# Optimization experiments

Measured on AMD Instinct MI355X. Metric: run time of the kernel, lower is better.

Reference implementation:

```python
import jax, jax.numpy as jnp
import numpy as np

B, FC, FRAMES, C = 8, 256, 512, 256


def conv1d(x, w, stride=1, pad=(0, 0), dil=1):
    # x: [N, Cin, L], w: [Cout, Cin, K]
    return jax.lax.conv_general_dilated(
        x, w, window_strides=(stride,), padding=[pad],
        rhs_dilation=(dil,), dimension_numbers=('NCH', 'OIH', 'NCH'))


def setup_inputs() -> dict:
    key = jax.random.key(0)
    ks = jax.random.split(key, 8)
    s = 0.05
    x = jax.random.normal(ks[0], (B, FC, FRAMES), dtype=jnp.float32)
    enc_w0 = jax.random.normal(ks[1], (128, 1, 7), dtype=jnp.float32) * s
    enc_w123 = jax.random.normal(ks[2], (3, 128, 128, 7), dtype=jnp.float32) * s
    enc_w4567 = jax.random.normal(ks[3], (4, 128, 128, 3), dtype=jnp.float32) * s
    enc_w8 = jax.random.normal(ks[4], (C, 128, 1), dtype=jnp.float32) * s
    main_w = jax.random.normal(ks[5], (8, C, C, 2), dtype=jnp.float32) * s
    gate_w = jax.random.normal(ks[6], (8, C, C, 2), dtype=jnp.float32) * s
    judge_w = jax.random.normal(ks[7], (1, C, 1), dtype=jnp.float32) * s
    return {'x': x, 'enc_w0': enc_w0, 'enc_w123': enc_w123,
            'enc_w4567': enc_w4567, 'enc_w8': enc_w8,
            'main_w': main_w, 'gate_w': gate_w, 'judge_w': judge_w}


def reference(x, enc_w0, enc_w123, enc_w4567, enc_w8, main_w, gate_w, judge_w):
    lrelu = lambda h: jax.nn.leaky_relu(h, 0.2)
    b = x.shape[0]
    # [B, FC, FRAMES] -> [B*FRAMES, 1, FC]: encode each frame's feature vector
    h = jnp.transpose(x, (0, 2, 1)).reshape(-1, 1, FC)
    h = lrelu(conv1d(h, enc_w0, stride=2, pad=(3, 3)))
    for i in range(3):
        h = lrelu(conv1d(h, enc_w123[i], stride=2, pad=(3, 3)))
    for i in range(4):
        h = lrelu(conv1d(h, enc_w4567[i], stride=2, pad=(1, 1)))
    h = conv1d(h, enc_w8)                       # [B*FRAMES, C, 1], no activation
    h = jnp.transpose(h.reshape(b, FRAMES, C), (0, 2, 1))  # [B, C, FRAMES]
    # WaveNet stack: causal pad + dilated k=2 convs + tanh*sigmoid gate + residual
    feats = jnp.zeros_like(h)
    for i in range(8):
        p = 2 ** i
        z = jnp.tanh(conv1d(h, main_w[i], pad=(p, 0), dil=p)) * \
            jax.nn.sigmoid(conv1d(h, gate_w[i], pad=(p, 0), dil=p))
        feats = feats + z
        h = z + h                              # channels always match -> residual
    latent = feats
    j = conv1d(latent, judge_w)[:, :, -1:]      # [B, 1, 1]
    return latent[:, :, -1:], j
```

## Files before the change

kernel.cpp:

```cpp
#include <hip/hip_runtime.h>
#include <math.h>

#define FC 256
#define NB 8
#define RS 136

typedef __attribute__((ext_vector_type(8))) _Float16 f16x8;
typedef __attribute__((ext_vector_type(4))) float f32x4;

__device__ __forceinline__ float lrelu(float v) { return fmaxf(v, 0.2f * v); }
__device__ __forceinline__ unsigned short f2h(float f) {
  _Float16 h = (_Float16)f;
  return *(unsigned short*)&h;
}
__device__ __forceinline__ void bar() { asm volatile("s_barrier" ::: "memory"); }
__device__ __forceinline__ void wait_lgkm0() { asm volatile("s_waitcnt lgkmcnt(0)" ::: "memory"); }

#define N1 344064
#define N2 196608
#define N3 32768
#define NTOT 573440
#define NWN 2097152

__global__ void pack_kernel(const float* __restrict__ w123,
                            const float* __restrict__ w4567,
                            const float* __restrict__ w8,
                            const float* __restrict__ mw,
                            const float* __restrict__ gw,
                            unsigned short* __restrict__ wp,
                            unsigned short* __restrict__ wn) {
  int idx = blockIdx.x * 512 + threadIdx.x;
  if (idx < N1) {
    int e = idx & 7, lane = (idx >> 3) & 63, ct = (idx >> 9) & 7, ks = (idx >> 12) & 3, t = idx >> 14;
    int l = t / 7, kw = t % 7;
    int co = ct * 16 + (lane & 15), ci = ks * 32 + (lane >> 4) * 8 + e;
    wp[idx] = f2h(w123[(((l * 128 + co) * 128) + ci) * 7 + kw]);
  } else if (idx < N1 + N2) {
    int k = idx - N1;
    int e = k & 7, lane = (k >> 3) & 63, ct = (k >> 9) & 7, ks = (k >> 12) & 3, t = k >> 14;
    int l = t / 3, kw = t % 3;
    int co = ct * 16 + (lane & 15), ci = ks * 32 + (lane >> 4) * 8 + e;
    wp[idx] = f2h(w4567[(((l * 128 + co) * 128) + ci) * 3 + kw]);
  } else if (idx < NTOT) {
    int k = idx - N1 - N2;
    int e = k & 7, lane = (k >> 3) & 63, ct = (k >> 9) & 15, ks = (k >> 13) & 3;
    int co = ct * 16 + (lane & 15), ci = ks * 32 + (lane >> 4) * 8 + e;
    wp[idx] = f2h(w8[co * 128 + ci]);
  } else if (idx < NTOT + NWN) {
    int k2 = idx - NTOT;
    int li = k2 >> 18, w = k2 & 262143;
    int e = w & 7, lane = (w >> 3) & 63, rt = (w >> 9) & 31, k32 = w >> 14;
    int row = rt * 16 + (lane & 15), k = k32 * 32 + (lane >> 4) * 8 + e;
    int ch = row >> 1, mat = row & 1, kw = k >> 8, ci = k & 255;
    const float* src = mat ? gw : mw;
    wn[k2] = f2h(src[(((size_t)li * 256 + ch) * 256 + ci) * 2 + kw]);
  }
}

template<int KW, int POFF, int PIN, int POUT, int MC, int MN, int OM>
__device__ __forceinline__ void mlayer_d(const unsigned short* __restrict__ wp,
                                         const unsigned short* __restrict__ sin_,
                                         unsigned short* __restrict__ sout,
                                         unsigned short* __restrict__ gact,
                                         int tid, int frame) {
  constexpr int HRIN = PIN / 2 + 4;
  constexpr int HROUT = POUT / 2 + 4;
  constexpr int Nt = (POUT + 15) / 16;
  constexpr int MNg = Nt / MN;
  constexpr int MCg = 8 / MNg;
  static_assert(MC * MCg == 8, "cout tiling must cover 128 channels");
  constexpr int NS = KW * 4;
  constexpr int DA = NS < 6 ? NS : 6;
  constexpr int DB = MC == 1 ? (NS < 4 ? NS : 4) : (NS < 3 ? NS : 3);

  const int wid = tid >> 6, lane = tid & 63, nl = lane & 15, q = lane >> 4;
  const int mcg = wid / MNg, mng = wid % MNg;
  const int ct0 = mcg * MC, nt0 = mng * MN;

  int jj[MN]; bool val[MN]; int rofs[MN][KW];
#pragma unroll
  for (int jn = 0; jn < MN; ++jn) {
    int n = (nt0 + jn) * 16 + nl;
    val[jn] = (n < POUT);
    jj[jn] = val[jn] ? n : 0;
#pragma unroll
    for (int kw = 0; kw < KW; ++kw) {
      int P = 2 * jj[jn] + kw - POFF + 4;
      rofs[jn][kw] = ((P & 1) * HRIN + (P >> 1)) * RS + q * 8;
    }
  }
  const unsigned short* wl = wp + (size_t)ct0 * 512 + lane * 8;

  f32x4 acc[MC][MN];
#pragma unroll
  for (int i = 0; i < MC; ++i)
#pragma unroll
    for (int jn = 0; jn < MN; ++jn) acc[i][jn] = (f32x4){0.f, 0.f, 0.f, 0.f};

  f16x8 A[DA][MC], B[DB][MN];
#pragma unroll
  for (int s = 0; s < DA; ++s)
#pragma unroll
    for (int i = 0; i < MC; ++i)
      A[s][i] = *(const f16x8*)(wl + (size_t)s * 4096 + i * 512);
#pragma unroll
  for (int s = 0; s < DB; ++s) {
    const int kw = s >> 2, ks = s & 3;
#pragma unroll
    for (int jn = 0; jn < MN; ++jn)
      B[s][jn] = *(const f16x8*)(sin_ + rofs[jn][kw] + ks * 32);
  }
#pragma unroll
  for (int s = 0; s < NS; ++s) {
    const int sa = s % DA, sb = s % DB;
#pragma unroll
    for (int i = 0; i < MC; ++i)
#pragma unroll
      for (int jn = 0; jn < MN; ++jn)
        acc[i][jn] = __builtin_amdgcn_mfma_f32_16x16x32_f16(A[sa][i], B[sb][jn], acc[i][jn], 0, 0, 0);
    if (s + DA < NS) {
#pragma unroll
      for (int i = 0; i < MC; ++i)
        A[sa][i] = *(const f16x8*)(wl + (size_t)(s + DA) * 4096 + i * 512);
    }
    if (s + DB < NS) {
      const int kw = (s + DB) >> 2, ks = (s + DB) & 3;
#pragma unroll
      for (int jn = 0; jn < MN; ++jn)
        B[sb][jn] = *(const f16x8*)(sin_ + rofs[jn][kw] + ks * 32);
    }
  }

#pragma unroll
  for (int i = 0; i < MC; ++i) {
#pragma unroll
    for (int jn = 0; jn < MN; ++jn) {
      if (!val[jn]) continue;
      unsigned int lo = (unsigned)f2h(lrelu(acc[i][jn][0])) | ((unsigned)f2h(lrelu(acc[i][jn][1])) << 16);
      unsigned int hi = (unsigned)f2h(lrelu(acc[i][jn][2])) | ((unsigned)f2h(lrelu(acc[i][jn][3])) << 16);
      const int j = jj[jn];
      if (OM == 1) {
        *(uint2*)(gact + ((size_t)frame * POUT + j) * 128 + (ct0 + i) * 16 + q * 4) = make_uint2(lo, hi);
      } else {
        const int row = (j & 1) * HROUT + (j >> 1) + 2;
        *(uint2*)(sout + (size_t)row * RS + (ct0 + i) * 16 + q * 4) = make_uint2(lo, hi);
      }
    }
  }
  if (OM == 0) {
    constexpr int DEND = ((POUT - 1) >> 1) + 3;
    constexpr int NZ = 2 + (HROUT - DEND);
    unsigned int* zp = (unsigned int*)sout;
    for (int s2 = tid; s2 < 2 * NZ * 68; s2 += 512) {
      int col = s2 % 68, rr = s2 / 68;
      int par = rr / NZ, rz = rr % NZ;
      int row = rz < 2 ? rz : DEND + rz - 2;
      zp[((size_t)par * HROUT + row) * 68 + col] = 0;
    }
    __syncthreads();
  }
}

__global__ __launch_bounds__(512, 4)
void encoder1(const float* __restrict__ x, const float* __restrict__ w0,
              const unsigned short* __restrict__ wp123,
              const unsigned short* __restrict__ wp4,
              unsigned short* __restrict__ act4g) {
  __shared__ __align__(16) unsigned short actA[18496];
  __shared__ __align__(16) unsigned short actB[9792];
  float* s_x = (float*)actB;
  const int tid = threadIdx.x;
  const int frame = blockIdx.x;
  const int bb = frame >> 8;
  const int t = (frame & 255) + 256;

  if (tid < 256) s_x[3 + tid] = x[((bb << 8) + tid) * 512 + t];
  else if (tid < 259) s_x[tid - 256] = 0.f;
  else if (tid < 262) s_x[tid] = 0.f;
  wait_lgkm0();
  bar();

  {
    const int c = tid & 127;
    const int half = tid >> 7;
    float wv[7];
#pragma unroll
    for (int k = 0; k < 7; ++k) wv[k] = w0[c * 7 + k];
    for (int j = half * 32; j < half * 32 + 32; ++j) {
      float s = 0.f;
#pragma unroll
      for (int k = 0; k < 7; ++k) s += wv[k] * s_x[2 * j + k];
      int row = ((j & 1) ? 68 : 0) + (j >> 1) + 2;
      actA[row * RS + c] = f2h(lrelu(s));
    }
    unsigned int* zp = (unsigned int*)actA;
    for (int s2 = tid; s2 < 2 * 4 * 68; s2 += 512) {
      int col = s2 % 68;
      int rr = s2 / 68;
      int par = rr >> 2, r2 = rr & 3;
      int row = (r2 < 2) ? r2 : (64 + r2);
      zp[((size_t)par * 68 + row) * 68 + col] = 0;
    }
  }
  wait_lgkm0();
  bar();

  mlayer_d<7, 3, 128, 64, 2, 2, 0>(wp123,          actA, actB, nullptr, tid, frame);
  mlayer_d<7, 3, 64, 32, 1, 2, 0>(wp123 + 114688,  actB, actA, nullptr, tid, frame);
  mlayer_d<7, 3, 32, 16, 1, 1, 0>(wp123 + 229376,  actA, actA + 5440, nullptr, tid, frame);
  mlayer_d<3, 1, 16, 8, 1, 1, 1>(wp4,              actA + 5440, nullptr, act4g, tid, frame);
}

template<int KW, int POFF, int PIN, int POUT, int FPB, int COUT, int MC, int MN, int OM, bool FLATIN>
__device__ __forceinline__ void mlayer(const unsigned short* __restrict__ wp,
                                       const unsigned short* __restrict__ sin_,
                                       unsigned short* __restrict__ sout,
                                       float* __restrict__ gout,
                                       int tid, int frame0) {
  constexpr int HRIN  = PIN / 2 + 4;
  constexpr int HROUT = POUT / 2 + 4;
  constexpr int NVAL = POUT * FPB;
  constexpr int Nt = (NVAL + 15) / 16;
  constexpr int Ct = COUT / 16;
  constexpr int MCg = Ct / MC, MNg = Nt / MN;
  constexpr int KS = 4;
  constexpr int NS = KW * KS;
  constexpr int DA = NS < 6 ? NS : 6;
  constexpr int DB = NS < 3 ? NS : 3;
  constexpr int L2P = POUT == 1 ? 0 : POUT == 2 ? 1 : POUT == 4 ? 2 : POUT == 8 ? 3 :
                      POUT == 16 ? 4 : POUT == 32 ? 5 : 6;

  const int wid = tid >> 6, lane = tid & 63, nl = lane & 15, q = lane >> 4;

  for (int mac = wid; mac < MCg * MNg; mac += 8) {
    const int mcg = mac / MNg, mng = mac % MNg;
    const int ct0 = mcg * MC, nt0 = mng * MN;
    int jj[MN]; bool val[MN];
#pragma unroll
    for (int jn = 0; jn < MN; ++jn) {
      int n = (nt0 + jn) * 16 + nl;
      val[jn] = (n < NVAL);
      jj[jn] = val[jn] ? n : 0;
    }
    int rofs[MN][KW];
#pragma unroll
    for (int jn = 0; jn < MN; ++jn) {
      const int f = jj[jn] >> L2P, j = jj[jn] & (POUT - 1);
#pragma unroll
      for (int kw = 0; kw < KW; ++kw) {
        if (FLATIN) {
          rofs[jn][kw] = jj[jn] * RS + q * 8;
        } else {
          int P = 2 * j + kw - POFF + 4;
          rofs[jn][kw] = (f * 2 * HRIN + (P & 1) * HRIN + (P >> 1)) * RS + q * 8;
        }
      }
    }
    int abase[MC];
#pragma unroll
    for (int i = 0; i < MC; ++i) abase[i] = (ct0 + i) * 512 + lane * 8;

    f32x4 acc[MC][MN];
#pragma unroll
    for (int i = 0; i < MC; ++i)
#pragma unroll
      for (int jn = 0; jn < MN; ++jn) acc[i][jn] = (f32x4){0.f, 0.f, 0.f, 0.f};

    f16x8 A[DA][MC], B[DB][MN];
#pragma unroll
    for (int s = 0; s < DA; ++s) {
      const int kw = s / KS, ks = s % KS;
#pragma unroll
      for (int i = 0; i < MC; ++i)
        A[s][i] = *(const f16x8*)(wp + (size_t)(kw * KS + ks) * (Ct * 512) + abase[i]);
    }
#pragma unroll
    for (int s = 0; s < DB; ++s) {
      const int kw = s / KS, ks = s % KS;
#pragma unroll
      for (int jn = 0; jn < MN; ++jn)
        B[s][jn] = *(const f16x8*)(sin_ + rofs[jn][kw] + ks * 32);
    }
#pragma unroll
    for (int s = 0; s < NS; ++s) {
      const int sa = s % DA, sb = s % DB;
#pragma unroll
      for (int i = 0; i < MC; ++i)
#pragma unroll
        for (int jn = 0; jn < MN; ++jn)
          acc[i][jn] = __builtin_amdgcn_mfma_f32_16x16x32_f16(A[sa][i], B[sb][jn], acc[i][jn], 0, 0, 0);
      if (s + DA < NS) {
        const int kw = (s + DA) / KS, ks = (s + DA) % KS;
#pragma unroll
        for (int i = 0; i < MC; ++i)
          A[sa][i] = *(const f16x8*)(wp + (size_t)(kw * KS + ks) * (Ct * 512) + abase[i]);
      }
      if (s + DB < NS) {
        const int kw = (s + DB) / KS, ks = (s + DB) % KS;
#pragma unroll
        for (int jn = 0; jn < MN; ++jn)
          B[sb][jn] = *(const f16x8*)(sin_ + rofs[jn][kw] + ks * 32);
      }
    }
#pragma unroll
    for (int i = 0; i < MC; ++i) {
#pragma unroll
      for (int jn = 0; jn < MN; ++jn) {
        if (OM == 3) {
          if (val[jn]) {
            const int frame = frame0 + jj[jn];
            float4 v = make_float4(acc[i][jn][0], acc[i][jn][1], acc[i][jn][2], acc[i][jn][3]);
            *(float4*)(gout + (size_t)frame * 256 + (ct0 + i) * 16 + q * 4) = v;
          }
        } else if (OM == 2) {
          if (val[jn]) {
            unsigned int lo = (unsigned)f2h(lrelu(acc[i][jn][0])) | ((unsigned)f2h(lrelu(acc[i][jn][1])) << 16);
            unsigned int hi = (unsigned)f2h(lrelu(acc[i][jn][2])) | ((unsigned)f2h(lrelu(acc[i][jn][3])) << 16);
            *(uint2*)(sout + (size_t)jj[jn] * RS + (ct0 + i) * 16 + q * 4) = make_uint2(lo, hi);
          }
        } else {
          if (val[jn]) {
            const int f = jj[jn] >> L2P, j = jj[jn] & (POUT - 1);
            const int row = f * 2 * HROUT + (j & 1) * HROUT + (j >> 1) + 2;
            unsigned int lo = (unsigned)f2h(lrelu(acc[i][jn][0])) | ((unsigned)f2h(lrelu(acc[i][jn][1])) << 16);
            unsigned int hi = (unsigned)f2h(lrelu(acc[i][jn][2])) | ((unsigned)f2h(lrelu(acc[i][jn][3])) << 16);
            *(uint2*)(sout + (size_t)row * RS + (ct0 + i) * 16 + q * 4) = make_uint2(lo, hi);
          }
        }
      }
    }
  }
  if (OM == 0) {
    constexpr int DEND = ((POUT - 1) >> 1) + 3;
    constexpr int NZ = 2 + (HROUT - DEND);
    constexpr int TOTU = FPB * 2 * NZ * (RS / 2);
    unsigned int* zp = (unsigned int*)sout;
    for (int s2 = tid; s2 < TOTU; s2 += 512) {
      int col = s2 % 68;
      int rr = s2 / 68;
      int fr = rr / (2 * NZ), r2 = rr % (2 * NZ);
      int par = r2 / NZ, rz = r2 % NZ;
      int row = rz < 2 ? rz : DEND + rz - 2;
      zp[((size_t)(fr * 2 + par) * HROUT + row) * 68 + col] = 0;
    }
    __syncthreads();
  } else if (OM == 2) {
    __syncthreads();
  }
}

__global__ __launch_bounds__(512)
void encoder2(const unsigned short* __restrict__ act4g,
              const unsigned short* __restrict__ wp4,
              const unsigned short* __restrict__ wp8,
              float* __restrict__ h) {
  __shared__ __align__(16) unsigned short actP[17408];
  __shared__ __align__(16) unsigned short actQ[13056];
  __shared__ __align__(16) unsigned short actR[2176];
  const int tid = threadIdx.x;
  const int frame0 = blockIdx.x * 8;

  {
    uint4 z4 = make_uint4(0, 0, 0, 0);
    for (int s = tid; s < 2176; s += 512) ((uint4*)actP)[s] = z4;
    for (int s = tid; s < 1632; s += 512) ((uint4*)actQ)[s] = z4;
    for (int s = tid; s < 272; s += 512) ((uint4*)actR)[s] = z4;
  }
  __syncthreads();
  for (int c = tid; c < 1024; c += 512) {
    int f = c >> 7, rem = c & 127, pos = rem >> 4, o = (rem & 15) * 8;
    uint4 v = *(const uint4*)(act4g + ((size_t)(frame0 + f) * 8 + pos) * 128 + o);
    int P = pos + 4;
    int row = (P & 1) * 8 + (P >> 1);
    *(uint4*)(actP + ((size_t)f * 16 + row) * RS + o) = v;
  }
  __syncthreads();

  mlayer<3, 1, 8, 4, 8, 128, 2, 1, 0, false>(wp4 + 49152,  actP, actQ, nullptr, tid, frame0);
  mlayer<3, 1, 4, 2, 8, 128, 1, 1, 0, false>(wp4 + 98304,  actQ, actP, nullptr, tid, frame0);
  mlayer<3, 1, 2, 1, 8, 128, 1, 1, 2, false>(wp4 + 147456, actP, actR, nullptr, tid, frame0);
  mlayer<1, 0, 1, 1, 8, 256, 1, 1, 3, true>(wp8,           actR, nullptr, h, tid, frame0);
}

__global__ __launch_bounds__(256)
void wnet_kernel(const unsigned short* __restrict__ wn,
                 const float* __restrict__ hsrc, float* __restrict__ hdst,
                 float* __restrict__ feats, const float* __restrict__ jw,
                 float* __restrict__ out, int li) {
  const int npos = 128 >> li, p = 1 << li, N = npos * 8, lnp = 7 - li;
  const int tid = threadIdx.x;
  const int nb = blockIdx.x >> 2, mb = blockIdx.x & 3;
  const int n0 = nb * 16;
  __shared__ __align__(16) unsigned short sB[16 * 520];
  __shared__ float jls[8];

  for (int c = tid; c < 1024; c += 256) {
    const int nr = c >> 6, o = (c & 63) * 8;
    const int n = n0 + nr;
    unsigned short tmp[8] = {0, 0, 0, 0, 0, 0, 0, 0};
    if (n < N) {
      const int b = n >> lnp, kk = n & (npos - 1);
      const int t = 255 - (kk << (li + 1));
      const float* src = (o < 256) ? hsrc + ((size_t)(b * 256 + t - p)) * 256 + o
                                   : hsrc + ((size_t)(b * 256 + t)) * 256 + (o - 256);
#pragma unroll
      for (int e = 0; e < 8; ++e) tmp[e] = f2h(src[e]);
    }
    unsigned int u0 = (unsigned)tmp[0] | ((unsigned)tmp[1] << 16);
    unsigned int u1 = (unsigned)tmp[2] | ((unsigned)tmp[3] << 16);
    unsigned int u2 = (unsigned)tmp[4] | ((unsigned)tmp[5] << 16);
    unsigned int u3 = (unsigned)tmp[6] | ((unsigned)tmp[7] << 16);
    *(uint4*)(sB + (size_t)nr * 520 + o) = make_uint4(u0, u1, u2, u3);
  }
  __syncthreads();

  const int wid = tid >> 6, lane = tid & 63, nl = lane & 15, q = lane >> 4;
  f32x4 acc[2];
  acc[0] = (f32x4){0.f, 0.f, 0.f, 0.f};
  acc[1] = (f32x4){0.f, 0.f, 0.f, 0.f};
  int arow[2];
#pragma unroll
  for (int i = 0; i < 2; ++i) arow[i] = (mb * 8 + wid * 2 + i) * 512 + lane * 8;
  const int bofs = nl * 520 + q * 8;

  f16x8 A[4][2], Bv[2];
#pragma unroll
  for (int s = 0; s < 4; ++s)
#pragma unroll
    for (int i = 0; i < 2; ++i) A[s][i] = *(const f16x8*)(wn + arow[i] + (size_t)s * 16384);
#pragma unroll
  for (int s = 0; s < 2; ++s) Bv[s] = *(const f16x8*)(sB + bofs + s * 32);
#pragma unroll
  for (int s = 0; s < 16; ++s) {
    const int sa = s & 3, sb = s & 1;
    acc[0] = __builtin_amdgcn_mfma_f32_16x16x32_f16(A[sa][0], Bv[sb], acc[0], 0, 0, 0);
    acc[1] = __builtin_amdgcn_mfma_f32_16x16x32_f16(A[sa][1], Bv[sb], acc[1], 0, 0, 0);
    if (s + 4 < 16) {
#pragma unroll
      for (int i = 0; i < 2; ++i) A[sa][i] = *(const f16x8*)(wn + arow[i] + (size_t)(s + 4) * 16384);
    }
    if (s + 2 < 16) Bv[sb] = *(const f16x8*)(sB + bofs + (s + 2) * 32);
  }

  const int n = n0 + nl;
  if (li < 7) {
    if (n < N) {
      const int b = n >> lnp, kk = n & (npos - 1);
      const int t = 255 - (kk << (li + 1));
      const size_t rowoff = ((size_t)(b * 256 + t)) * 256;
#pragma unroll
      for (int i = 0; i < 2; ++i) {
        const int ch = mb * 64 + (wid * 2 + i) * 8 + q * 2;
        const float z0 = tanhf(acc[i][0]) * (1.f / (1.f + expf(-acc[i][1])));
        const float z1 = tanhf(acc[i][2]) * (1.f / (1.f + expf(-acc[i][3])));
        float2 hv = *(const float2*)(hsrc + rowoff + ch);
        *(float2*)(hdst + rowoff + ch) = make_float2(hv.x + z0, hv.y + z1);
        if (kk == 0) {
          float* fp = feats + b * 256 + ch;
          if (li == 0) { fp[0] = z0; fp[1] = z1; }
          else         { fp[0] += z0; fp[1] += z1; }
        }
      }
    }
  } else {
    if (tid < 8) jls[tid] = 0.f;
    __syncthreads();
    if (n < N) {
      const int b = n;
      float partial = 0.f;
#pragma unroll
      for (int i = 0; i < 2; ++i) {
        const int ch = mb * 64 + (wid * 2 + i) * 8 + q * 2;
        const float z0 = tanhf(acc[i][0]) * (1.f / (1.f + expf(-acc[i][1])));
        const float z1 = tanhf(acc[i][2]) * (1.f / (1.f + expf(-acc[i][3])));
        const float* fp = feats + b * 256 + ch;
        const float f0 = fp[0] + z0;
        const float f1 = fp[1] + z1;
        *(float2*)(out + b * 256 + ch) = make_float2(f0, f1);
        partial += f0 * jw[ch] + f1 * jw[ch + 1];
      }
      atomicAdd(&jls[b], partial);
    }
    __syncthreads();
    if (tid < 8) atomicAdd(out + NB * 256 + tid, jls[tid]);
  }
}

extern "C" void kernel_launch(void* const* d_in, const int* in_sizes, int n_in,
                              void* d_out, int out_size, void* d_ws, size_t ws_size,
                              hipStream_t stream) {
  const float* x     = (const float*)d_in[0];
  const float* w0    = (const float*)d_in[1];
  const float* w123  = (const float*)d_in[2];
  const float* w4567 = (const float*)d_in[3];
  const float* w8    = (const float*)d_in[4];
  const float* mw    = (const float*)d_in[5];
  const float* gw    = (const float*)d_in[6];
  const float* jw    = (const float*)d_in[7];
  float* out = (float*)d_out;

  float* ws = (float*)d_ws;
  unsigned short* act4g = (unsigned short*)ws;
  float* h0    = ws + 1048576;
  float* h1    = ws + 1572864;
  float* feats = ws + 2097152;
  unsigned short* wp = (unsigned short*)(ws + 2099200);
  unsigned short* wn = (unsigned short*)(ws + 2385920);

  hipMemsetAsync(out + NB * 256, 0, NB * sizeof(float), stream);
  pack_kernel<<<5216, 512, 0, stream>>>(w123, w4567, w8, mw, gw, wp, wn);
  encoder1<<<2048, 512, 0, stream>>>(x, w0, wp, wp + N1, act4g);
  encoder2<<<256, 512, 0, stream>>>(act4g, wp + N1, wp + N1 + N2, h0);

  float* hs = h0; float* hd = h1;
  for (int i = 0; i < 8; ++i) {
    const unsigned short* wl = wn + (size_t)i * 262144;
    const int N = (128 >> i) * 8;
    const int nN = (N + 15) / 16;
    wnet_kernel<<<4 * nN, 256, 0, stream>>>(wl, hs, hd, feats, jw, out, i);
    float* tmp = hd; hd = hs; hs = tmp;
  }
}
```

Baseline: 218.3 us.

## Process two frames per encoder1 block to reuse weight fragments

encoder1 now handles two frames per block. Each weight A-fragment loaded from global memory feeds MFMAs for both frames, and the LDS activation buffers are doubled. The grid is halved and launch bounds are dropped to 2 blocks per CU, which trades occupancy and more registers for halved weight traffic. Separately, the wnet_kernel staging loop now reads its input with float4 vector loads instead of scalar loads.

```diff
diff --git a/kernel.cpp b/kernel.cpp
--- a/kernel.cpp
+++ b/kernel.cpp
@@ -58,11 +58,13 @@
 }
 
 template<int KW, int POFF, int PIN, int POUT, int MC, int MN, int OM>
-__device__ __forceinline__ void mlayer_d(const unsigned short* __restrict__ wp,
-                                         const unsigned short* __restrict__ sin_,
-                                         unsigned short* __restrict__ sout,
-                                         unsigned short* __restrict__ gact,
-                                         int tid, int frame) {
+__device__ __forceinline__ void mlayer_d2(const unsigned short* __restrict__ wp,
+                                          const unsigned short* __restrict__ sin0,
+                                          const unsigned short* __restrict__ sin1,
+                                          unsigned short* __restrict__ sout0,
+                                          unsigned short* __restrict__ sout1,
+                                          unsigned short* __restrict__ gact,
+                                          int tid, int frame0) {
   constexpr int HRIN = PIN / 2 + 4;
   constexpr int HROUT = POUT / 2 + 4;
   constexpr int Nt = (POUT + 15) / 16;
@@ -71,11 +73,14 @@
   static_assert(MC * MCg == 8, "cout tiling must cover 128 channels");
   constexpr int NS = KW * 4;
   constexpr int DA = NS < 6 ? NS : 6;
-  constexpr int DB = MC == 1 ? (NS < 4 ? NS : 4) : (NS < 3 ? NS : 3);
+  constexpr int DB = NS < 3 ? NS : 3;
 
   const int wid = tid >> 6, lane = tid & 63, nl = lane & 15, q = lane >> 4;
   const int mcg = wid / MNg, mng = wid % MNg;
   const int ct0 = mcg * MC, nt0 = mng * MN;
+
+  const unsigned short* sins[2] = {sin0, sin1};
+  unsigned short* souts[2] = {sout0, sout1};
 
   int jj[MN]; bool val[MN]; int rofs[MN][KW];
 #pragma unroll
@@ -91,13 +96,15 @@
   }
   const unsigned short* wl = wp + (size_t)ct0 * 512 + lane * 8;
 
-  f32x4 acc[MC][MN];
+  f32x4 acc[MC][MN][2];
 #pragma unroll
   for (int i = 0; i < MC; ++i)
 #pragma unroll
-    for (int jn = 0; jn < MN; ++jn) acc[i][jn] = (f32x4){0.f, 0.f, 0.f, 0.f};
-
-  f16x8 A[DA][MC], B[DB][MN];
+    for (int jn = 0; jn < MN; ++jn)
+#pragma unroll
+      for (int f = 0; f < 2; ++f) acc[i][jn][f] = (f32x4){0.f, 0.f, 0.f, 0.f};
+
+  f16x8 A[DA][MC], B[DB][MN][2];
 #pragma unroll
   for (int s = 0; s < DA; ++s)
 #pragma unroll
@@ -108,7 +115,9 @@
     const int kw = s >> 2, ks = s & 3;
 #pragma unroll
     for (int jn = 0; jn < MN; ++jn)
-      B[s][jn] = *(const f16x8*)(sin_ + rofs[jn][kw] + ks * 32);
+#pragma unroll
+      for (int f = 0; f < 2; ++f)
+        B[s][jn][f] = *(const f16x8*)(sins[f] + rofs[jn][kw] + ks * 32);
   }
 #pragma unroll
   for (int s = 0; s < NS; ++s) {
@@ -117,7 +126,9 @@
     for (int i = 0; i < MC; ++i)
 #pragma unroll
       for (int jn = 0; jn < MN; ++jn)
-        acc[i][jn] = __builtin_amdgcn_mfma_f32_16x16x32_f16(A[sa][i], B[sb][jn], acc[i][jn], 0, 0, 0);
+#pragma unroll
+        for (int f = 0; f < 2; ++f)
+          acc[i][jn][f] = __builtin_amdgcn_mfma_f32_16x16x32_f16(A[sa][i], B[sb][jn][f], acc[i][jn][f], 0, 0, 0);
     if (s + DA < NS) {
 #pragma unroll
       for (int i = 0; i < MC; ++i)
@@ -127,88 +138,111 @@
       const int kw = (s + DB) >> 2, ks = (s + DB) & 3;
 #pragma unroll
       for (int jn = 0; jn < MN; ++jn)
-        B[sb][jn] = *(const f16x8*)(sin_ + rofs[jn][kw] + ks * 32);
-    }
-  }
-
-#pragma unroll
-  for (int i = 0; i < MC; ++i) {
-#pragma unroll
-    for (int jn = 0; jn < MN; ++jn) {
-      if (!val[jn]) continue;
-      unsigned int lo = (unsigned)f2h(lrelu(acc[i][jn][0])) | ((unsigned)f2h(lrelu(acc[i][jn][1])) << 16);
-      unsigned int hi = (unsigned)f2h(lrelu(acc[i][jn][2])) | ((unsigned)f2h(lrelu(acc[i][jn][3])) << 16);
-      const int j = jj[jn];
-      if (OM == 1) {
-        *(uint2*)(gact + ((size_t)frame * POUT + j) * 128 + (ct0 + i) * 16 + q * 4) = make_uint2(lo, hi);
-      } else {
-        const int row = (j & 1) * HROUT + (j >> 1) + 2;
-        *(uint2*)(sout + (size_t)row * RS + (ct0 + i) * 16 + q * 4) = make_uint2(lo, hi);
+#pragma unroll
+        for (int f = 0; f < 2; ++f)
+          B[sb][jn][f] = *(const f16x8*)(sins[f] + rofs[jn][kw] + ks * 32);
+    }
+  }
+
+#pragma unroll
+  for (int f = 0; f < 2; ++f) {
+#pragma unroll
+    for (int i = 0; i < MC; ++i) {
+#pragma unroll
+      for (int jn = 0; jn < MN; ++jn) {
+        if (!val[jn]) continue;
+        unsigned int lo = (unsigned)f2h(lrelu(acc[i][jn][f][0])) | ((unsigned)f2h(lrelu(acc[i][jn][f][1])) << 16);
+        unsigned int hi = (unsigned)f2h(lrelu(acc[i][jn][f][2])) | ((unsigned)f2h(lrelu(acc[i][jn][f][3])) << 16);
+        const int j = jj[jn];
+        if (OM == 1) {
+          *(uint2*)(gact + ((size_t)(frame0 + f) * POUT + j) * 128 + (ct0 + i) * 16 + q * 4) = make_uint2(lo, hi);
+        } else {
+          const int row = (j & 1) * HROUT + (j >> 1) + 2;
+          *(uint2*)(souts[f] + (size_t)row * RS + (ct0 + i) * 16 + q * 4) = make_uint2(lo, hi);
+        }
       }
     }
   }
   if (OM == 0) {
     constexpr int DEND = ((POUT - 1) >> 1) + 3;
     constexpr int NZ = 2 + (HROUT - DEND);
-    unsigned int* zp = (unsigned int*)sout;
-    for (int s2 = tid; s2 < 2 * NZ * 68; s2 += 512) {
-      int col = s2 % 68, rr = s2 / 68;
-      int par = rr / NZ, rz = rr % NZ;
-      int row = rz < 2 ? rz : DEND + rz - 2;
-      zp[((size_t)par * HROUT + row) * 68 + col] = 0;
+#pragma unroll
+    for (int f = 0; f < 2; ++f) {
+      unsigned int* zp = (unsigned int*)souts[f];
+      for (int s2 = tid; s2 < 2 * NZ * 68; s2 += 512) {
+        int col = s2 % 68, rr = s2 / 68;
+        int par = rr / NZ, rz = rr % NZ;
+        int row = rz < 2 ? rz : DEND + rz - 2;
+        zp[((size_t)par * HROUT + row) * 68 + col] = 0;
+      }
     }
     __syncthreads();
   }
 }
 
-__global__ __launch_bounds__(512, 4)
+__global__ __launch_bounds__(512, 2)
 void encoder1(const float* __restrict__ x, const float* __restrict__ w0,
               const unsigned short* __restrict__ wp123,
               const unsigned short* __restrict__ wp4,
               unsigned short* __restrict__ act4g) {
-  __shared__ __align__(16) unsigned short actA[18496];
-  __shared__ __align__(16) unsigned short actB[9792];
-  float* s_x = (float*)actB;
+  __shared__ __align__(16) unsigned short actA[2 * 18496];
+  __shared__ __align__(16) unsigned short actB[2 * 9792];
   const int tid = threadIdx.x;
-  const int frame = blockIdx.x;
-  const int bb = frame >> 8;
-  const int t = (frame & 255) + 256;
-
-  if (tid < 256) s_x[3 + tid] = x[((bb << 8) + tid) * 512 + t];
-  else if (tid < 259) s_x[tid - 256] = 0.f;
-  else if (tid < 262) s_x[tid] = 0.f;
+  const int frame0 = blockIdx.x * 2;
+  const int bb = frame0 >> 8;
+  const int t0 = (frame0 & 255) + 256;
+
+  float* s_x0 = (float*)actB;
+  float* s_x1 = (float*)actB + 272;
+
+  if (tid < 256) s_x0[3 + tid] = x[((bb << 8) + tid) * 512 + t0];
+  else           s_x1[3 + (tid & 255)] = x[((bb << 8) + (tid & 255)) * 512 + t0 + 1];
+  if (tid < 3)                 { s_x0[tid] = 0.f; s_x1[tid] = 0.f; }
+  if (tid >= 259 && tid < 262) { s_x0[tid] = 0.f; s_x1[tid] = 0.f; }
   wait_lgkm0();
   bar();
 
   {
     const int c = tid & 127;
-    const int half = tid >> 7;
+    const int sel = tid >> 7;
     float wv[7];
 #pragma unroll
     for (int k = 0; k < 7; ++k) wv[k] = w0[c * 7 + k];
-    for (int j = half * 32; j < half * 32 + 32; ++j) {
-      float s = 0.f;
-#pragma unroll
-      for (int k = 0; k < 7; ++k) s += wv[k] * s_x[2 * j + k];
-      int row = ((j & 1) ? 68 : 0) + (j >> 1) + 2;
-      actA[row * RS + c] = f2h(lrelu(s));
-    }
-    unsigned int* zp = (unsigned int*)actA;
-    for (int s2 = tid; s2 < 2 * 4 * 68; s2 += 512) {
-      int col = s2 % 68;
-      int rr = s2 / 68;
-      int par = rr >> 2, r2 = rr & 3;
-      int row = (r2 < 2) ? r2 : (64 + r2);
-      zp[((size_t)par * 68 + row) * 68 + col] = 0;
+#pragma unroll
+    for (int f = 0; f < 2; ++f) {
+      const float* sx = f ? s_x1 : s_x0;
+      unsigned short* aA = actA + f * 18496;
+      for (int j = sel * 32; j < sel * 32 + 32; ++j) {
+        float s = 0.f;
+#pragma unroll
+        for (int k = 0; k < 7; ++k) s += wv[k] * sx[2 * j + k];
+        int row = ((j & 1) ? 68 : 0) + (j >> 1) + 2;
+        aA[row * RS + c] = f2h(lrelu(s));
+      }
+    }
+#pragma unroll
+    for (int f = 0; f < 2; ++f) {
+      unsigned int* zp = (unsigned int*)(actA + f * 18496);
+      for (int s2 = tid; s2 < 2 * 4 * 68; s2 += 512) {
+        int col = s2 % 68;
+        int rr = s2 / 68;
+        int par = rr >> 2, r2 = rr & 3;
+        int row = (r2 < 2) ? r2 : (64 + r2);
+        zp[((size_t)par * 68 + row) * 68 + col] = 0;
+      }
     }
   }
   wait_lgkm0();
   bar();
 
-  mlayer_d<7, 3, 128, 64, 2, 2, 0>(wp123,          actA, actB, nullptr, tid, frame);
-  mlayer_d<7, 3, 64, 32, 1, 2, 0>(wp123 + 114688,  actB, actA, nullptr, tid, frame);
-  mlayer_d<7, 3, 32, 16, 1, 1, 0>(wp123 + 229376,  actA, actA + 5440, nullptr, tid, frame);
-  mlayer_d<3, 1, 16, 8, 1, 1, 1>(wp4,              actA + 5440, nullptr, act4g, tid, frame);
+  mlayer_d2<7, 3, 128, 64, 2, 2, 0>(wp123,         actA, actA + 18496, actB, actB + 9792,
+                                    nullptr, tid, frame0);
+  mlayer_d2<7, 3, 64, 32, 1, 2, 0>(wp123 + 114688, actB, actB + 9792, actA, actA + 18496,
+                                    nullptr, tid, frame0);
+  mlayer_d2<7, 3, 32, 16, 1, 1, 0>(wp123 + 229376, actA, actA + 18496,
+                                    actA + 5440, actA + 18496 + 5440, nullptr, tid, frame0);
+  mlayer_d2<3, 1, 16, 8, 1, 1, 1>(wp4,             actA + 5440, actA + 18496 + 5440,
+                                    nullptr, nullptr, act4g, tid, frame0);
 }
 
 template<int KW, int POFF, int PIN, int POUT, int FPB, int COUT, int MC, int MN, int OM, bool FLATIN>
@@ -403,8 +437,10 @@
       const int t = 255 - (kk << (li + 1));
       const float* src = (o < 256) ? hsrc + ((size_t)(b * 256 + t - p)) * 256 + o
                                    : hsrc + ((size_t)(b * 256 + t)) * 256 + (o - 256);
-#pragma unroll
-      for (int e = 0; e < 8; ++e) tmp[e] = f2h(src[e]);
+      float4 v0 = *(const float4*)(src);
+      float4 v1 = *(const float4*)(src + 4);
+      tmp[0] = f2h(v0.x); tmp[1] = f2h(v0.y); tmp[2] = f2h(v0.z); tmp[3] = f2h(v0.w);
+      tmp[4] = f2h(v1.x); tmp[5] = f2h(v1.y); tmp[6] = f2h(v1.z); tmp[7] = f2h(v1.w);
     }
     unsigned int u0 = (unsigned)tmp[0] | ((unsigned)tmp[1] << 16);
     unsigned int u1 = (unsigned)tmp[2] | ((unsigned)tmp[3] << 16);
@@ -509,7 +545,7 @@
 
   hipMemsetAsync(out + NB * 256, 0, NB * sizeof(float), stream);
   pack_kernel<<<5216, 512, 0, stream>>>(w123, w4567, w8, mw, gw, wp, wn);
-  encoder1<<<2048, 512, 0, stream>>>(x, w0, wp, wp + N1, act4g);
+  encoder1<<<1024, 512, 0, stream>>>(x, w0, wp, wp + N1, act4g);
   encoder2<<<256, 512, 0, stream>>>(act4g, wp + N1, wp + N1 + N2, h0);
 
   float* hs = h0; float* hd = h1;
```

After: 212.7 us. -2.6%, faster.
